# Kernel tuning notes

Hardware: AMD Instinct MI355X
Metric: run time of the kernel (lower is better)

The kernel has to match this reference:

```python
import jax, jax.numpy as jnp
import numpy as np
import math

B, T, NQ, NK, D, H = 2, 4, 576, 576, 1024, 16
DH = D // H  # 64 per-head dim
N_POS = (24, 20, 20)          # temporal, y, x rope splits (sum = DH)
CUTOFFS = (256.0, 256.0, 256.0)
CUTOFF_SPATIAL = 0.5
NEG = float(np.finfo(np.float32).min) / 2.0


def _rotate_half(x):
    s = x.shape
    xr = x.reshape(s[:-1] + (s[-1] // 2, 2))
    x1, x2 = xr[..., 0], xr[..., 1]
    return jnp.stack((-x2, x1), axis=-1).reshape(s)


def _co_si(coords, freqs):
    # coords: [B,T,N,3]; freqs[a]: [1,1,n_a/2]
    # NOTE: torch code's scale = 1/sqrt(len(freq)) evaluates to 1.0 since
    # len(param of shape [1,1,n/2]) == 1; we faithfully omit it.
    cos_parts, sin_parts = [], []
    for a, f in enumerate(freqs):
        arg = 0.5 * math.pi * coords[..., a:a + 1] * f[0, 0]  # [B,T,N,n_a/2]
        cos_parts.append(jnp.cos(arg))
        sin_parts.append(jnp.sin(arg))
    return jnp.concatenate(cos_parts, -1), jnp.concatenate(sin_parts, -1)


def _lin(x, W, b):
    # torch nn.Linear: y = x @ W.T + b, W:[out,in]
    return jnp.einsum('...i,oi->...o', x, W) + b


def setup_inputs() -> dict:
    key = jax.random.key(0)
    ks = jax.random.split(key, 16)
    sc = 0.02
    inp = {
        'q_tokens': jax.random.normal(ks[0], (B, T, NQ, D), jnp.float32),
        'kv_tokens': jax.random.normal(ks[1], (B, T, NK, D), jnp.float32),
        'coords_q': jax.random.uniform(ks[2], (B, T, NQ, 3), jnp.float32),
        'coords_k': jax.random.uniform(ks[3], (B, T, NK, 3), jnp.float32),
        'q_pad_mask': jax.random.randint(ks[4], (B, T, NQ), 0, 2).astype(bool),
        'kv_pad_mask': jax.random.randint(ks[5], (B, T, NK), 0, 2).astype(bool),
        'Wq': jax.random.normal(ks[6], (D, D), jnp.float32) * sc,
        'bq': jax.random.normal(ks[7], (D,), jnp.float32) * sc,
        'Wk': jax.random.normal(ks[8], (D, D), jnp.float32) * sc,
        'bk': jax.random.normal(ks[9], (D,), jnp.float32) * sc,
        'Wv': jax.random.normal(ks[10], (D, D), jnp.float32) * sc,
        'bv': jax.random.normal(ks[11], (D,), jnp.float32) * sc,
        'Wo': jax.random.normal(ks[12], (D, D), jnp.float32) * sc,
        'bo': jax.random.normal(ks[13], (D,), jnp.float32) * sc,
        'alpha': jax.random.normal(ks[14], (H,), jnp.float32) * 0.1,
    }
    for i, (c, n) in enumerate(zip(CUTOFFS, N_POS)):
        inp[f'freq{i}'] = jnp.exp(jnp.linspace(0.0, -math.log(c), n // 2)).reshape(1, 1, -1).astype(jnp.float32)
    return inp


def reference(q_tokens, kv_tokens, coords_q, coords_k, q_pad_mask, kv_pad_mask,
              Wq, bq, Wk, bk, Wv, bv, Wo, bo, alpha, freq0, freq1, freq2):
    freqs = (freq0, freq1, freq2)
    # projections -> [B,H,T,N,d]
    q = _lin(q_tokens, Wq, bq).reshape(B, T, NQ, H, DH).transpose(0, 3, 1, 2, 4)
    k = _lin(kv_tokens, Wk, bk).reshape(B, T, NK, H, DH).transpose(0, 3, 1, 2, 4)
    v = _lin(kv_tokens, Wv, bv).reshape(B, T, NK, H, DH).transpose(0, 3, 1, 2, 4)
    # 4D RoPE
    co_q, si_q = _co_si(coords_q, freqs)
    co_k, si_k = _co_si(coords_k, freqs)
    co_q = jnp.repeat(co_q, 2, axis=-1)[:, None]  # [B,1,T,Nq,d]
    si_q = jnp.repeat(si_q, 2, axis=-1)[:, None]
    co_k = jnp.repeat(co_k, 2, axis=-1)[:, None]
    si_k = jnp.repeat(si_k, 2, axis=-1)[:, None]
    q = q * co_q + _rotate_half(q) * si_q
    k = k * co_k + _rotate_half(k) * si_k
    # spatial cdist on (y,x) = last two coord dims -> [B,T,Nq,Nk]
    diff = coords_q[:, :, :, None, 1:] - coords_k[:, :, None, :, 1:]
    dist = jnp.sqrt(jnp.sum(diff * diff, axis=-1))
    bias = jnp.where(dist > CUTOFF_SPATIAL, NEG, 0.0)[:, None]           # cutoff mask
    prior = jnp.exp(-5.0 * dist / CUTOFF_SPATIAL)[:, None]               # v1 distance prior
    bias = bias + alpha[None, :, None, None, None] * prior               # [B,H,T,Nq,Nk]
    ignore = (q_pad_mask[..., :, None] | kv_pad_mask[..., None, :])[:, None]
    bias = jnp.where(ignore, NEG, bias)
    # SDPA per frame
    scores = jnp.einsum('bhtqd,bhtkd->bhtqk', q, k) / math.sqrt(DH) + bias
    attn = jax.nn.softmax(scores, axis=-1)
    y = jnp.einsum('bhtqk,bhtkd->bhtqd', attn, v)
    y = y.transpose(0, 2, 3, 1, 4).reshape(B, T, NQ, D)
    return _lin(y, Wo, bo)
```

## Files before the change

kernel.cpp:

```cpp
#include <hip/hip_runtime.h>
#include <math.h>
#include <stdint.h>

#define BB 2
#define TT 4
#define NQ 576
#define NKV 576
#define DD 1024
#define HH 16
#define DH 64
#define BT (BB*TT)
#define NTOK (BT*NQ)
#define NPAIR ((size_t)BT*NQ*NKV)
#define NEGV (-(3.402823466e38f) * 0.5f)

typedef __attribute__((ext_vector_type(8))) short short8v;
typedef __attribute__((ext_vector_type(4))) float f32x4;

__device__ inline ushort f2bf(float f) {
    union { float f; uint32_t u; } v; v.f = f;
    return (ushort)((v.u + 0x7FFFu + ((v.u >> 16) & 1u)) >> 16);
}

__device__ inline void gld_lds16(const ushort* g, ushort* l) {
    __builtin_amdgcn_global_load_lds(
        (const __attribute__((address_space(1))) unsigned int*)g,
        (__attribute__((address_space(3))) unsigned int*)l, 16, 0, 0);
}

__global__ __launch_bounds__(256) void canon_masks_kernel(
    const uint8_t* __restrict__ qm_raw, const uint8_t* __restrict__ km_raw,
    uint8_t* __restrict__ qm_out, uint8_t* __restrict__ km_out)
{
    __shared__ int flag_s;
    const int tid = threadIdx.x;
    if (tid == 0) flag_s = 0;
    __syncthreads();
    int local = 0;
    for (int j = tid; j < NTOK; j += 256) {
        if ((j & 3) != 0 && (qm_raw[j] | km_raw[j])) local = 1;
    }
    if (local) atomicOr(&flag_s, 1);
    __syncthreads();
    const int is_u8 = flag_s;
    const int* qi32 = (const int*)qm_raw;
    const int* ki32 = (const int*)km_raw;
    for (int j = tid; j < NTOK; j += 256) {
        qm_out[j] = is_u8 ? qm_raw[j] : (uint8_t)(qi32[j] != 0);
        km_out[j] = is_u8 ? km_raw[j] : (uint8_t)(ki32[j] != 0);
    }
}

__global__ __launch_bounds__(256) void build_cs_kernel(
    const float* __restrict__ cq, const float* __restrict__ ck,
    const float* __restrict__ f0, const float* __restrict__ f1,
    const float* __restrict__ f2,
    float2* __restrict__ csq, float2* __restrict__ csk)
{
    const int PER = NTOK * 32;
    int idx = blockIdx.x * 256 + threadIdx.x;
    int half = idx / PER;
    int r = idx - half * PER;
    int i = r & 31;
    int tok = r >> 5;
    int axis; float f;
    if (i < 12)      { axis = 0; f = f0[i];      }
    else if (i < 22) { axis = 1; f = f1[i - 12]; }
    else             { axis = 2; f = f2[i - 22]; }
    const float* C = half ? ck : cq;
    float c = C[tok * 3 + axis];
    float arg = __fmul_rn(__fmul_rn(1.57079632679489662f, c), f);
    float s, co;
    __sincosf(arg, &s, &co);
    float2 out; out.x = co; out.y = s;
    (half ? csk : csq)[tok * 32 + i] = out;
}

__global__ __launch_bounds__(576) void prior_kernel(
    const float* __restrict__ cq, const float* __restrict__ ck,
    const uint8_t* __restrict__ qm, const uint8_t* __restrict__ km,
    float* __restrict__ prior, uint8_t* __restrict__ flagb)
{
    const int bq = blockIdx.x;
    const int kv = threadIdx.x;
    const int bt = bq / NQ;
    const float qy = cq[bq * 3 + 1], qx = cq[bq * 3 + 2];
    const int kb = bt * NKV + kv;
    const float ky = ck[kb * 3 + 1], kx = ck[kb * 3 + 2];
    float dy = __fsub_rn(qy, ky);
    float dx = __fsub_rn(qx, kx);
    float d2 = __fadd_rn(__fmul_rn(dy, dy), __fmul_rn(dx, dx));
    float dist = __fsqrt_rn(d2);
    int fl = (dist > 0.5f) | qm[bq] | km[kb];
    size_t o = (size_t)bq * NKV + kv;
    prior[o] = __expf(-10.f * dist);
    flagb[o] = (uint8_t)fl;
}

__global__ __launch_bounds__(256) void f2bf_kernel(
    const float* __restrict__ src, ushort* __restrict__ dst, int n4)
{
    int i = blockIdx.x * 256 + threadIdx.x;
    if (i < n4) {
        float4 v = ((const float4*)src)[i];
        ushort4 o;
        o.x = f2bf(v.x); o.y = f2bf(v.y); o.z = f2bf(v.z); o.w = f2bf(v.w);
        ((ushort4*)dst)[i] = o;
    }
}

__global__ __launch_bounds__(256) void gemm_bf16_kernel(
    const ushort* __restrict__ X, const ushort* __restrict__ W,
    const float* __restrict__ bias, void* __restrict__ O,
    const float2* __restrict__ cst, const int mode)
{
    __shared__ ushort As[64 * 64];
    __shared__ ushort Bs[128 * 64];
    const int tid = threadIdx.x;
    const int bid = blockIdx.x;
    const int m0 = (bid >> 3) * 64, n0 = (bid & 7) * 128;
    const int lane = tid & 63, w = tid >> 6;
    const int wm = (w & 1) * 32, wn = (w >> 1) * 64;
    const int frow = lane & 15, quad = lane >> 4;
    const int srow = lane >> 3;
    const int scole = ((lane & 7) ^ srow) << 3;

    f32x4 acc[2][4];
#pragma unroll
    for (int m = 0; m < 2; m++)
#pragma unroll
        for (int n = 0; n < 4; n++) acc[m][n] = (f32x4)0.f;

    for (int k0 = 0; k0 < DD; k0 += 64) {
        __syncthreads();
#pragma unroll
        for (int j = 0; j < 2; j++) {
            int c = w * 2 + j;
            gld_lds16(&X[(size_t)(m0 + c * 8 + srow) * DD + k0 + scole], &As[c * 512]);
        }
#pragma unroll
        for (int j = 0; j < 4; j++) {
            int c = w * 4 + j;
            gld_lds16(&W[(size_t)(n0 + c * 8 + srow) * DD + k0 + scole], &Bs[c * 512]);
        }
        __syncthreads();
        const int rsw = (frow & 7) << 3;
#pragma unroll
        for (int ks = 0; ks < 2; ks++) {
            short8v a[2], b[4];
#pragma unroll
            for (int m = 0; m < 2; m++)
                a[m] = *(const short8v*)&As[(wm + m * 16 + frow) * 64 + ((ks * 32 + quad * 8) ^ rsw)];
#pragma unroll
            for (int n = 0; n < 4; n++)
                b[n] = *(const short8v*)&Bs[(wn + n * 16 + frow) * 64 + ((ks * 32 + quad * 8) ^ rsw)];
#pragma unroll
            for (int m = 0; m < 2; m++)
#pragma unroll
                for (int n = 0; n < 4; n++)
                    acc[m][n] = __builtin_amdgcn_mfma_f32_16x16x32_bf16(
                        a[m], b[n], acc[m][n], 0, 0, 0);
        }
    }

#pragma unroll
    for (int m = 0; m < 2; m++) {
        const int gr0 = m0 + wm + m * 16 + quad * 4;
#pragma unroll
        for (int n = 0; n < 4; n++) {
            const int gc = n0 + wn + n * 16 + frow;
            const float bv_ = bias[gc];
            f32x4 c = acc[m][n];
            if (mode == 1) {
#pragma unroll
                for (int i = 0; i < 4; i++)
                    ((float*)O)[(size_t)(gr0 + i) * DD + gc] = c[i] + bv_;
            } else if (mode == 3) {
                int bt = gr0 / NQ, nn0 = gr0 - bt * NQ;
                int h = gc >> 6, dh = gc & 63;
                ushort4 o4;
                o4.x = f2bf(c[0] + bv_); o4.y = f2bf(c[1] + bv_);
                o4.z = f2bf(c[2] + bv_); o4.w = f2bf(c[3] + bv_);
                *(ushort4*)&((ushort*)O)[(((size_t)(bt * HH + h)) * DH + dh) * NQ + nn0] = o4;
            } else {
                int h = gc >> 6, dh = gc & 63;
                int i2 = dh >> 1;
#pragma unroll
                for (int i = 0; i < 4; i++) {
                    int tok = gr0 + i;
                    float v = c[i] + bv_;
                    float vp = __shfl_xor(v, 1);
                    float2 cs = cst[tok * 32 + i2];
                    float o = (gc & 1) ? (v * cs.x + vp * cs.y)
                                       : (v * cs.x - vp * cs.y);
                    int bt = tok / NQ, nn = tok - bt * NQ;
                    ((ushort*)O)[(((size_t)(bt * HH + h)) * NQ + nn) * DH + dh] = f2bf(o);
                }
            }
        }
    }
}

__global__ __launch_bounds__(256) void attn_mfma_kernel(
    const ushort* __restrict__ Qh, const ushort* __restrict__ Kh,
    const ushort* __restrict__ Vtg,
    const float* __restrict__ prior, const uint8_t* __restrict__ flagb,
    const float* __restrict__ alpha, ushort* __restrict__ Yh)
{
    __shared__ ushort Ks[64][72];
    __shared__ ushort Vt[64][72];
    __shared__ ushort Ps[4][16][88];

    const int tid = threadIdx.x;
    const int lane = tid & 63, w = tid >> 6;
    const int quad = lane >> 4, l15 = lane & 15;

    int zz = blockIdx.y;
    const int b = zz >> 6; zz &= 63;
    const int h = zz >> 2; const int t = zz & 3;
    const int bt = b * TT + t;
    const int q0 = blockIdx.x * 64;

    const size_t hb = ((size_t)(bt * HH + h)) * NQ * DH;
    const size_t vb = ((size_t)(bt * HH + h)) * DH * NQ;
    const int qg = q0 + w * 16 + l15;

    const ushort* qrow = Qh + hb + (size_t)qg * DH;
    short8v qf0 = *(const short8v*)(qrow + quad * 8);
    short8v qf1 = *(const short8v*)(qrow + 32 + quad * 8);

    const float alph = alpha[h];
    const size_t pbase = ((size_t)(bt * NQ + qg)) * NKV;

    float m_run = -INFINITY, l_run = 0.f;
    f32x4 oacc[4];
#pragma unroll
    for (int i = 0; i < 4; i++) oacc[i] = (f32x4)0.f;

    for (int kt = 0; kt < 9; kt++) {
        const int k0 = kt * 64;
        __syncthreads();
        {
            int kv = tid >> 2, c = (tid & 3) * 16;
            const ushort* src = Kh + hb + (size_t)(k0 + kv) * DH + c;
            *(short8v*)&Ks[kv][c]     = *(const short8v*)(src);
            *(short8v*)&Ks[kv][c + 8] = *(const short8v*)(src + 8);
        }
        {
            int dh = tid >> 2, c = (tid & 3) * 16;
            const ushort* src = Vtg + vb + (size_t)dh * NQ + k0 + c;
            *(short8v*)&Vt[dh][c]     = *(const short8v*)(src);
            *(short8v*)&Vt[dh][c + 8] = *(const short8v*)(src + 8);
        }
        __syncthreads();

        f32x4 sc[4];
#pragma unroll
        for (int jt = 0; jt < 4; jt++) sc[jt] = (f32x4)0.f;
#pragma unroll
        for (int jt = 0; jt < 4; jt++) {
            short8v kf0 = *(const short8v*)&Ks[jt * 16 + l15][quad * 8];
            short8v kf1 = *(const short8v*)&Ks[jt * 16 + l15][32 + quad * 8];
            sc[jt] = __builtin_amdgcn_mfma_f32_16x16x32_bf16(kf0, qf0, sc[jt], 0, 0, 0);
            sc[jt] = __builtin_amdgcn_mfma_f32_16x16x32_bf16(kf1, qf1, sc[jt], 0, 0, 0);
        }

        float p[16];
        float mloc = -INFINITY;
#pragma unroll
        for (int jt = 0; jt < 4; jt++) {
            const size_t po = pbase + k0 + jt * 16 + quad * 4;
            float4 pr = *(const float4*)&prior[po];
            uchar4 fv = *(const uchar4*)&flagb[po];
#pragma unroll
            for (int r = 0; r < 4; r++) {
                float prv = (r == 0) ? pr.x : (r == 1) ? pr.y : (r == 2) ? pr.z : pr.w;
                uint8_t fl = (r == 0) ? fv.x : (r == 1) ? fv.y : (r == 2) ? fv.z : fv.w;
                float s = sc[jt][r] * 0.125f + (fl ? NEGV : alph * prv);
                p[jt * 4 + r] = s;
                mloc = fmaxf(mloc, s);
            }
        }
        mloc = fmaxf(mloc, __shfl_xor(mloc, 16));
        mloc = fmaxf(mloc, __shfl_xor(mloc, 32));
        float m_new = fmaxf(m_run, mloc);
        float scale = __expf(m_run - m_new);
        float psum = 0.f;
#pragma unroll
        for (int i = 0; i < 16; i++) {
            float pv = __expf(p[i] - m_new);
            p[i] = pv;
            psum += pv;
        }
        psum += __shfl_xor(psum, 16);
        psum += __shfl_xor(psum, 32);
        l_run = l_run * scale + psum;
        m_run = m_new;

        float sr[4];
#pragma unroll
        for (int r = 0; r < 4; r++) sr[r] = __shfl(scale, quad * 4 + r);
#pragma unroll
        for (int tdh = 0; tdh < 4; tdh++)
#pragma unroll
            for (int r = 0; r < 4; r++) oacc[tdh][r] *= sr[r];

#pragma unroll
        for (int jt = 0; jt < 4; jt++) {
#pragma unroll
            for (int rp = 0; rp < 2; rp++) {
                uint32_t pk = (uint32_t)f2bf(p[jt * 4 + 2 * rp]) |
                              ((uint32_t)f2bf(p[jt * 4 + 2 * rp + 1]) << 16);
                *(uint32_t*)&Ps[w][l15][jt * 16 + quad * 4 + 2 * rp] = pk;
            }
        }

        short8v pa0 = *(const short8v*)&Ps[w][l15][quad * 8];
        short8v pa1 = *(const short8v*)&Ps[w][l15][32 + quad * 8];
#pragma unroll
        for (int tdh = 0; tdh < 4; tdh++) {
            short8v vb0 = *(const short8v*)&Vt[tdh * 16 + l15][quad * 8];
            short8v vb1 = *(const short8v*)&Vt[tdh * 16 + l15][32 + quad * 8];
            oacc[tdh] = __builtin_amdgcn_mfma_f32_16x16x32_bf16(pa0, vb0, oacc[tdh], 0, 0, 0);
            oacc[tdh] = __builtin_amdgcn_mfma_f32_16x16x32_bf16(pa1, vb1, oacc[tdh], 0, 0, 0);
        }
    }

    float linv = 1.0f / l_run;
    float li[4];
#pragma unroll
    for (int r = 0; r < 4; r++) li[r] = __shfl(linv, quad * 4 + r);
#pragma unroll
    for (int tdh = 0; tdh < 4; tdh++) {
#pragma unroll
        for (int r = 0; r < 4; r++) {
            int tok = bt * NQ + q0 + w * 16 + quad * 4 + r;
            Yh[(size_t)tok * DD + h * DH + tdh * 16 + l15] = f2bf(oacc[tdh][r] * li[r]);
        }
    }
}

extern "C" void kernel_launch(void* const* d_in, const int* in_sizes, int n_in,
                              void* d_out, int out_size, void* d_ws, size_t ws_size,
                              hipStream_t stream)
{
    const float*   q_tokens  = (const float*)d_in[0];
    const float*   kv_tokens = (const float*)d_in[1];
    const float*   coords_q  = (const float*)d_in[2];
    const float*   coords_k  = (const float*)d_in[3];
    const uint8_t* q_pad     = (const uint8_t*)d_in[4];
    const uint8_t* kv_pad    = (const uint8_t*)d_in[5];
    const float*   Wq = (const float*)d_in[6];
    const float*   bq = (const float*)d_in[7];
    const float*   Wk = (const float*)d_in[8];
    const float*   bk = (const float*)d_in[9];
    const float*   Wv = (const float*)d_in[10];
    const float*   bv = (const float*)d_in[11];
    const float*   Wo = (const float*)d_in[12];
    const float*   bo = (const float*)d_in[13];
    const float*   alpha = (const float*)d_in[14];
    const float*   f0 = (const float*)d_in[15];
    const float*   f1 = (const float*)d_in[16];
    const float*   f2 = (const float*)d_in[17];
    float* out = (float*)d_out;

    const size_t SZ = (size_t)NTOK * DD;
    const size_t WSZ = (size_t)DD * DD;
    float2*  csq  = (float2*)d_ws;
    float2*  csk  = csq + (size_t)NTOK * 32;
    float*   prior = (float*)(csk + (size_t)NTOK * 32);
    ushort*  qtb  = (ushort*)(prior + NPAIR);
    ushort*  ktb  = qtb + SZ;
    ushort*  Wqb  = ktb + SZ;
    ushort*  Wkb  = Wqb + WSZ;
    ushort*  Wvb  = Wkb + WSZ;
    ushort*  Wob  = Wvb + WSZ;
    ushort*  Qh   = Wob + WSZ;
    ushort*  Kh   = Qh + SZ;
    ushort*  Vtg  = Kh + SZ;
    ushort*  Yh   = Vtg + SZ;
    uint8_t* flagb = (uint8_t*)(Yh + SZ);
    uint8_t* qm_c = flagb + NPAIR;
    uint8_t* km_c = qm_c + NTOK;

    canon_masks_kernel<<<1, 256, 0, stream>>>(q_pad, kv_pad, qm_c, km_c);

    build_cs_kernel<<<(2 * NTOK * 32) / 256, 256, 0, stream>>>(
        coords_q, coords_k, f0, f1, f2, csq, csk);

    prior_kernel<<<NTOK, 576, 0, stream>>>(
        coords_q, coords_k, qm_c, km_c, prior, flagb);

    f2bf_kernel<<<(int)(SZ / 4 / 256), 256, 0, stream>>>(q_tokens,  qtb, (int)(SZ / 4));
    f2bf_kernel<<<(int)(SZ / 4 / 256), 256, 0, stream>>>(kv_tokens, ktb, (int)(SZ / 4));
    f2bf_kernel<<<(int)(WSZ / 4 / 256), 256, 0, stream>>>(Wq, Wqb, (int)(WSZ / 4));
    f2bf_kernel<<<(int)(WSZ / 4 / 256), 256, 0, stream>>>(Wk, Wkb, (int)(WSZ / 4));
    f2bf_kernel<<<(int)(WSZ / 4 / 256), 256, 0, stream>>>(Wv, Wvb, (int)(WSZ / 4));
    f2bf_kernel<<<(int)(WSZ / 4 / 256), 256, 0, stream>>>(Wo, Wob, (int)(WSZ / 4));

    const int NBLK = (NTOK / 64) * (DD / 128);
    gemm_bf16_kernel<<<NBLK, 256, 0, stream>>>(qtb, Wqb, bq, Qh,  csq, 4);
    gemm_bf16_kernel<<<NBLK, 256, 0, stream>>>(ktb, Wkb, bk, Kh,  csk, 5);
    gemm_bf16_kernel<<<NBLK, 256, 0, stream>>>(ktb, Wvb, bv, Vtg, nullptr, 3);

    attn_mfma_kernel<<<dim3(9, BB * HH * TT), 256, 0, stream>>>(
        Qh, Kh, Vtg, prior, flagb, alpha, Yh);

    gemm_bf16_kernel<<<NBLK, 256, 0, stream>>>(Yh, Wob, bo, out, nullptr, 1);
}
```

Baseline: 311.9 us.

## Fuse launches, remap blocks per XCD, and register-prefetch K/V and prior in attention

Folds mask canonicalization into the prior kernel and merges the six bf16 conversion launches into one. Merges the Q/K/V projection GEMMs into a single launch. Remaps block indices so neighbouring tiles share an XCD, for L2 locality in the GEMMs and attention. The attention kernel now prefetches the next K/V tile and the prior/flag values into registers while computing the current tile, overlapping global loads with MFMA work. The cost is higher register pressure and a redundant mask scan in every prior block.

```diff
diff --git a/kernel.cpp b/kernel.cpp
--- a/kernel.cpp
+++ b/kernel.cpp
@@ -26,29 +26,6 @@
     __builtin_amdgcn_global_load_lds(
         (const __attribute__((address_space(1))) unsigned int*)g,
         (__attribute__((address_space(3))) unsigned int*)l, 16, 0, 0);
-}
-
-__global__ __launch_bounds__(256) void canon_masks_kernel(
-    const uint8_t* __restrict__ qm_raw, const uint8_t* __restrict__ km_raw,
-    uint8_t* __restrict__ qm_out, uint8_t* __restrict__ km_out)
-{
-    __shared__ int flag_s;
-    const int tid = threadIdx.x;
-    if (tid == 0) flag_s = 0;
-    __syncthreads();
-    int local = 0;
-    for (int j = tid; j < NTOK; j += 256) {
-        if ((j & 3) != 0 && (qm_raw[j] | km_raw[j])) local = 1;
-    }
-    if (local) atomicOr(&flag_s, 1);
-    __syncthreads();
-    const int is_u8 = flag_s;
-    const int* qi32 = (const int*)qm_raw;
-    const int* ki32 = (const int*)km_raw;
-    for (int j = tid; j < NTOK; j += 256) {
-        qm_out[j] = is_u8 ? qm_raw[j] : (uint8_t)(qi32[j] != 0);
-        km_out[j] = is_u8 ? km_raw[j] : (uint8_t)(ki32[j] != 0);
-    }
 }
 
 __global__ __launch_bounds__(256) void build_cs_kernel(
@@ -78,47 +55,71 @@
 
 __global__ __launch_bounds__(576) void prior_kernel(
     const float* __restrict__ cq, const float* __restrict__ ck,
-    const uint8_t* __restrict__ qm, const uint8_t* __restrict__ km,
+    const uint8_t* __restrict__ qm_raw, const uint8_t* __restrict__ km_raw,
     float* __restrict__ prior, uint8_t* __restrict__ flagb)
 {
+    __shared__ int flag_s;
+    const int tid = threadIdx.x;
+    if (tid == 0) flag_s = 0;
+    __syncthreads();
+    int local = 0;
+    for (int j = tid; j < NTOK; j += 576) {
+        if ((j & 3) != 0 && (qm_raw[j] | km_raw[j])) local = 1;
+    }
+    if (local) atomicOr(&flag_s, 1);
+    __syncthreads();
+    const int is_u8 = flag_s;
+
     const int bq = blockIdx.x;
-    const int kv = threadIdx.x;
+    const int kv = tid;
     const int bt = bq / NQ;
+    const int kb = bt * NKV + kv;
+    uint8_t qmv = is_u8 ? qm_raw[bq] : (uint8_t)(((const int*)qm_raw)[bq] != 0);
+    uint8_t kmv = is_u8 ? km_raw[kb] : (uint8_t)(((const int*)km_raw)[kb] != 0);
     const float qy = cq[bq * 3 + 1], qx = cq[bq * 3 + 2];
-    const int kb = bt * NKV + kv;
     const float ky = ck[kb * 3 + 1], kx = ck[kb * 3 + 2];
     float dy = __fsub_rn(qy, ky);
     float dx = __fsub_rn(qx, kx);
     float d2 = __fadd_rn(__fmul_rn(dy, dy), __fmul_rn(dx, dx));
     float dist = __fsqrt_rn(d2);
-    int fl = (dist > 0.5f) | qm[bq] | km[kb];
+    int fl = (dist > 0.5f) | qmv | kmv;
     size_t o = (size_t)bq * NKV + kv;
     prior[o] = __expf(-10.f * dist);
     flagb[o] = (uint8_t)fl;
 }
 
-__global__ __launch_bounds__(256) void f2bf_kernel(
-    const float* __restrict__ src, ushort* __restrict__ dst, int n4)
+#define S4 ((int)((size_t)NTOK * DD / 4))
+#define W4 ((int)((size_t)DD * DD / 4))
+__global__ __launch_bounds__(256) void f2bf_all_kernel(
+    const float* __restrict__ q_tokens, const float* __restrict__ kv_tokens,
+    const float* __restrict__ Wq, const float* __restrict__ Wk,
+    const float* __restrict__ Wv, const float* __restrict__ Wo,
+    ushort* __restrict__ dst0)
 {
     int i = blockIdx.x * 256 + threadIdx.x;
-    if (i < n4) {
-        float4 v = ((const float4*)src)[i];
-        ushort4 o;
-        o.x = f2bf(v.x); o.y = f2bf(v.y); o.z = f2bf(v.z); o.w = f2bf(v.w);
-        ((ushort4*)dst)[i] = o;
-    }
-}
-
-__global__ __launch_bounds__(256) void gemm_bf16_kernel(
+    const float* src; int off;
+    if (i < 2 * S4) {
+        src = (i < S4) ? q_tokens : kv_tokens;
+        off = (i < S4) ? i : i - S4;
+    } else {
+        int j = i - 2 * S4;
+        int w = j >> 18;
+        src = (w == 0) ? Wq : (w == 1) ? Wk : (w == 2) ? Wv : Wo;
+        off = j & (W4 - 1);
+    }
+    float4 v = ((const float4*)src)[off];
+    ushort4 o;
+    o.x = f2bf(v.x); o.y = f2bf(v.y); o.z = f2bf(v.z); o.w = f2bf(v.w);
+    ((ushort4*)dst0)[i] = o;
+}
+
+__device__ __forceinline__ void gemm_core(
     const ushort* __restrict__ X, const ushort* __restrict__ W,
     const float* __restrict__ bias, void* __restrict__ O,
-    const float2* __restrict__ cst, const int mode)
-{
-    __shared__ ushort As[64 * 64];
-    __shared__ ushort Bs[128 * 64];
+    const float2* __restrict__ cst, const int mode,
+    const int m0, const int n0, ushort* As, ushort* Bs)
+{
     const int tid = threadIdx.x;
-    const int bid = blockIdx.x;
-    const int m0 = (bid >> 3) * 64, n0 = (bid & 7) * 128;
     const int lane = tid & 63, w = tid >> 6;
     const int wm = (w & 1) * 32, wn = (w >> 1) * 64;
     const int frow = lane & 15, quad = lane >> 4;
@@ -201,6 +202,45 @@
     }
 }
 
+__global__ __launch_bounds__(256) void gemm_proj3_kernel(
+    const ushort* __restrict__ qtb, const ushort* __restrict__ ktb,
+    const ushort* __restrict__ Wqb, const ushort* __restrict__ Wkb,
+    const ushort* __restrict__ Wvb,
+    const float* __restrict__ bq, const float* __restrict__ bk,
+    const float* __restrict__ bv,
+    ushort* __restrict__ Qh, ushort* __restrict__ Kh, ushort* __restrict__ Vtg,
+    const float2* __restrict__ csq, const float2* __restrict__ csk)
+{
+    __shared__ ushort As[64 * 64];
+    __shared__ ushort Bs[128 * 64];
+    const int L = blockIdx.x;
+    const int xcd = L & 7, j = L >> 3;
+    const int mt_g = xcd * 27 + (j >> 3);
+    const int nt = j & 7;
+    const int seg = mt_g / 72;
+    const int smt = mt_g - seg * 72;
+    const ushort* X = (seg == 0) ? qtb : ktb;
+    const ushort* W = (seg == 0) ? Wqb : (seg == 1) ? Wkb : Wvb;
+    const float* bias = (seg == 0) ? bq : (seg == 1) ? bk : bv;
+    void* O = (seg == 0) ? (void*)Qh : (seg == 1) ? (void*)Kh : (void*)Vtg;
+    const float2* cst = (seg == 0) ? csq : csk;
+    const int mode = (seg == 0) ? 4 : (seg == 1) ? 5 : 3;
+    gemm_core(X, W, bias, O, cst, mode, smt * 64, nt * 128, As, Bs);
+}
+
+__global__ __launch_bounds__(256) void gemm_out_kernel(
+    const ushort* __restrict__ Yh, const ushort* __restrict__ Wob,
+    const float* __restrict__ bo, float* __restrict__ out)
+{
+    __shared__ ushort As[64 * 64];
+    __shared__ ushort Bs[128 * 64];
+    const int L = blockIdx.x;
+    const int xcd = L & 7, j = L >> 3;
+    const int mt = xcd * 9 + (j >> 3);
+    const int nt = j & 7;
+    gemm_core(Yh, Wob, bo, (void*)out, nullptr, 1, mt * 64, nt * 128, As, Bs);
+}
+
 __global__ __launch_bounds__(256) void attn_mfma_kernel(
     const ushort* __restrict__ Qh, const ushort* __restrict__ Kh,
     const ushort* __restrict__ Vtg,
@@ -215,14 +255,16 @@
     const int lane = tid & 63, w = tid >> 6;
     const int quad = lane >> 4, l15 = lane & 15;
 
-    int zz = blockIdx.y;
-    const int b = zz >> 6; zz &= 63;
-    const int h = zz >> 2; const int t = zz & 3;
-    const int bt = b * TT + t;
-    const int q0 = blockIdx.x * 64;
+    const int L = blockIdx.x;
+    const int xcd = L & 7;
+    const int logical = xcd * 144 + (L >> 3);
+    const int bh = logical / 9;
+    const int qt = logical - bh * 9;
+    const int bt = bh >> 4, h = bh & 15;
+    const int q0 = qt * 64;
 
     const size_t hb = ((size_t)(bt * HH + h)) * NQ * DH;
-    const size_t vb = ((size_t)(bt * HH + h)) * DH * NQ;
+    const size_t vbs = ((size_t)(bt * HH + h)) * DH * NQ;
     const int qg = q0 + w * 16 + l15;
 
     const ushort* qrow = Qh + hb + (size_t)qg * DH;
@@ -230,7 +272,22 @@
     short8v qf1 = *(const short8v*)(qrow + 32 + quad * 8);
 
     const float alph = alpha[h];
-    const size_t pbase = ((size_t)(bt * NQ + qg)) * NKV;
+    const size_t pbase = ((size_t)(bt * NQ + qg)) * NKV + quad * 4;
+
+    const int krow = tid >> 2, kcol = (tid & 3) * 16;
+    const ushort* Ksrc = Kh + hb + (size_t)krow * DH + kcol;
+    const ushort* Vsrc = Vtg + vbs + (size_t)krow * NQ + kcol;
+
+    short8v ka0 = *(const short8v*)(Ksrc);
+    short8v ka1 = *(const short8v*)(Ksrc + 8);
+    short8v va0 = *(const short8v*)(Vsrc);
+    short8v va1 = *(const short8v*)(Vsrc + 8);
+    float4 prf[4]; uint32_t pfl[4];
+#pragma unroll
+    for (int jt = 0; jt < 4; jt++) {
+        prf[jt] = *(const float4*)&prior[pbase + jt * 16];
+        pfl[jt] = *(const uint32_t*)&flagb[pbase + jt * 16];
+    }
 
     float m_run = -INFINITY, l_run = 0.f;
     f32x4 oacc[4];
@@ -238,19 +295,18 @@
     for (int i = 0; i < 4; i++) oacc[i] = (f32x4)0.f;
 
     for (int kt = 0; kt < 9; kt++) {
-        const int k0 = kt * 64;
         __syncthreads();
-        {
-            int kv = tid >> 2, c = (tid & 3) * 16;
-            const ushort* src = Kh + hb + (size_t)(k0 + kv) * DH + c;
-            *(short8v*)&Ks[kv][c]     = *(const short8v*)(src);
-            *(short8v*)&Ks[kv][c + 8] = *(const short8v*)(src + 8);
-        }
-        {
-            int dh = tid >> 2, c = (tid & 3) * 16;
-            const ushort* src = Vtg + vb + (size_t)dh * NQ + k0 + c;
-            *(short8v*)&Vt[dh][c]     = *(const short8v*)(src);
-            *(short8v*)&Vt[dh][c + 8] = *(const short8v*)(src + 8);
+        *(short8v*)&Ks[krow][kcol]     = ka0;
+        *(short8v*)&Ks[krow][kcol + 8] = ka1;
+        *(short8v*)&Vt[krow][kcol]     = va0;
+        *(short8v*)&Vt[krow][kcol + 8] = va1;
+        if (kt < 8) {
+            const ushort* nk = Ksrc + (size_t)(kt + 1) * 64 * DH;
+            const ushort* nv = Vsrc + (size_t)(kt + 1) * 64;
+            ka0 = *(const short8v*)(nk);
+            ka1 = *(const short8v*)(nk + 8);
+            va0 = *(const short8v*)(nv);
+            va1 = *(const short8v*)(nv + 8);
         }
         __syncthreads();
 
@@ -269,16 +325,22 @@
         float mloc = -INFINITY;
 #pragma unroll
         for (int jt = 0; jt < 4; jt++) {
-            const size_t po = pbase + k0 + jt * 16 + quad * 4;
-            float4 pr = *(const float4*)&prior[po];
-            uchar4 fv = *(const uchar4*)&flagb[po];
 #pragma unroll
             for (int r = 0; r < 4; r++) {
-                float prv = (r == 0) ? pr.x : (r == 1) ? pr.y : (r == 2) ? pr.z : pr.w;
-                uint8_t fl = (r == 0) ? fv.x : (r == 1) ? fv.y : (r == 2) ? fv.z : fv.w;
+                float prv = (r == 0) ? prf[jt].x : (r == 1) ? prf[jt].y
+                          : (r == 2) ? prf[jt].z : prf[jt].w;
+                uint8_t fl = (uint8_t)(pfl[jt] >> (8 * r));
                 float s = sc[jt][r] * 0.125f + (fl ? NEGV : alph * prv);
                 p[jt * 4 + r] = s;
                 mloc = fmaxf(mloc, s);
+            }
+        }
+        if (kt < 8) {
+            const size_t nb = pbase + (size_t)(kt + 1) * 64;
+#pragma unroll
+            for (int jt = 0; jt < 4; jt++) {
+                prf[jt] = *(const float4*)&prior[nb + jt * 16];
+                pfl[jt] = *(const uint32_t*)&flagb[nb + jt * 16];
             }
         }
         mloc = fmaxf(mloc, __shfl_xor(mloc, 16));
@@ -380,31 +442,21 @@
     ushort*  Vtg  = Kh + SZ;
     ushort*  Yh   = Vtg + SZ;
     uint8_t* flagb = (uint8_t*)(Yh + SZ);
-    uint8_t* qm_c = flagb + NPAIR;
-    uint8_t* km_c = qm_c + NTOK;
-
-    canon_masks_kernel<<<1, 256, 0, stream>>>(q_pad, kv_pad, qm_c, km_c);
 
     build_cs_kernel<<<(2 * NTOK * 32) / 256, 256, 0, stream>>>(
         coords_q, coords_k, f0, f1, f2, csq, csk);
 
     prior_kernel<<<NTOK, 576, 0, stream>>>(
-        coords_q, coords_k, qm_c, km_c, prior, flagb);
-
-    f2bf_kernel<<<(int)(SZ / 4 / 256), 256, 0, stream>>>(q_tokens,  qtb, (int)(SZ / 4));
-    f2bf_kernel<<<(int)(SZ / 4 / 256), 256, 0, stream>>>(kv_tokens, ktb, (int)(SZ / 4));
-    f2bf_kernel<<<(int)(WSZ / 4 / 256), 256, 0, stream>>>(Wq, Wqb, (int)(WSZ / 4));
-    f2bf_kernel<<<(int)(WSZ / 4 / 256), 256, 0, stream>>>(Wk, Wkb, (int)(WSZ / 4));
-    f2bf_kernel<<<(int)(WSZ / 4 / 256), 256, 0, stream>>>(Wv, Wvb, (int)(WSZ / 4));
-    f2bf_kernel<<<(int)(WSZ / 4 / 256), 256, 0, stream>>>(Wo, Wob, (int)(WSZ / 4));
-
-    const int NBLK = (NTOK / 64) * (DD / 128);
-    gemm_bf16_kernel<<<NBLK, 256, 0, stream>>>(qtb, Wqb, bq, Qh,  csq, 4);
-    gemm_bf16_kernel<<<NBLK, 256, 0, stream>>>(ktb, Wkb, bk, Kh,  csk, 5);
-    gemm_bf16_kernel<<<NBLK, 256, 0, stream>>>(ktb, Wvb, bv, Vtg, nullptr, 3);
-
-    attn_mfma_kernel<<<dim3(9, BB * HH * TT), 256, 0, stream>>>(
+        coords_q, coords_k, q_pad, kv_pad, prior, flagb);
+
+    f2bf_all_kernel<<<(2 * S4 + 4 * W4) / 256, 256, 0, stream>>>(
+        q_tokens, kv_tokens, Wq, Wk, Wv, Wo, qtb);
+
+    gemm_proj3_kernel<<<1728, 256, 0, stream>>>(
+        qtb, ktb, Wqb, Wkb, Wvb, bq, bk, bv, Qh, Kh, Vtg, csq, csk);
+
+    attn_mfma_kernel<<<1152, 256, 0, stream>>>(
         Qh, Kh, Vtg, prior, flagb, alpha, Yh);
 
-    gemm_bf16_kernel<<<NBLK, 256, 0, stream>>>(Yh, Wob, bo, out, nullptr, 1);
-}
+    gemm_out_kernel<<<576, 256, 0, stream>>>(Yh, Wob, bo, out);
+}
```

New measurement: 259.1 us. 16.9% less time.
